# Kernel optimization log

Measured on AMD Instinct MI355X. Metric: run time of the kernel, lower is better.

Reference implementation:

```python
import jax, jax.numpy as jnp
import numpy as np

B, NODES, IN_DIM, OUT_DIM, CAPS, K, NUM_ROUTE = 32, 512, 256, 128, 16, 5, 3

def squash(s):
    # s: [..., out]; scale = |s|^2/(1+|s|^2), direction s/(|s|+eps)
    sn = jnp.sum(s * s, axis=-1, keepdims=True)
    return (sn / (1.0 + sn)) * s / (jnp.sqrt(sn) + 1e-8)

def setup_inputs() -> dict:
    key = jax.random.key(0)
    k1, k2, k3, k4 = jax.random.split(key, 4)
    return {
        "x": jax.random.normal(k1, (B, NODES, IN_DIM), jnp.float32),
        "contribution": jax.random.normal(k2, (B, NODES), jnp.float32),
        "W": jax.random.normal(k3, (K, IN_DIM, OUT_DIM), jnp.float32),
        "alpha": jax.random.normal(k4, (NODES, CAPS, K), jnp.float32),
    }

def reference(x, contribution, W, alpha):
    # per-node, per-capsule transform: sum_k alpha[n,c,k] * W[k,i,o] -> [nodes, caps, in, out]
    Wn = jnp.einsum('nck,kio->ncio', alpha, W)
    # prediction vectors u_hat: [B, caps, nodes, out]
    u_hat = jnp.einsum('bni,ncio->bcno', x, Wn)
    u_det = jax.lax.stop_gradient(u_hat)
    # routing logits b init from (detached) contribution: [B, caps, nodes, 1]
    b = jnp.broadcast_to(
        jax.lax.stop_gradient(contribution)[:, None, :, None],
        (x.shape[0], CAPS, x.shape[1], 1))
    for _ in range(NUM_ROUTE):
        c = jax.nn.softmax(b, axis=1)              # over capsule axis
        v = squash(jnp.sum(c * u_det, axis=2))     # [B, caps, out]
        b = b + jnp.einsum('bcno,bco->bcn', u_det, v)[..., None]
    c = jax.nn.softmax(b, axis=1)
    s = jnp.sum(c * u_hat, axis=2)                 # [B, caps, out] (non-detached)
    return squash(s)
```

## Files before the change

### kernel.cpp

```cpp
#include <hip/hip_runtime.h>
#include <math.h>

#define B_ 32
#define NODES_ 512
#define IN_ 256
#define OUT_ 128
#define CAPS_ 16
#define KW_ 5
#define M_ (B_*NODES_)
#define N_ (KW_*OUT_)
#define NCH 32

typedef __attribute__((ext_vector_type(8))) short short8;
typedef __attribute__((ext_vector_type(4))) float f32x4;

#define Y_BOFF   0
#define L_BOFF   41943040
#define V_BOFF   42991616
#define SP_BOFF  43253760
#define BT_SZ    (N_*IN_*2)

__device__ __forceinline__ float b2f(unsigned short u) {
  union { unsigned int i; float f; } c; c.i = ((unsigned int)u) << 16; return c.f;
}
__device__ __forceinline__ unsigned short f2b(float f) {
  union { float f; unsigned int i; } c; c.f = f;
  unsigned int u = c.i;
  u += 0x7fffu + ((u >> 16) & 1u);
  return (unsigned short)(u >> 16);
}
__device__ __forceinline__ void async_load16(const void* g, void* l) {
  __builtin_amdgcn_global_load_lds(
      (const __attribute__((address_space(1))) unsigned int*)g,
      (__attribute__((address_space(3))) unsigned int*)l, 16, 0, 0);
}

__global__ __launch_bounds__(256) void conv_w(const float* __restrict__ W,
                                              unsigned short* __restrict__ bThi,
                                              unsigned short* __restrict__ bTlo) {
  int n = blockIdx.x;
  int i = threadIdx.x;
  int k = n >> 7, o = n & 127;
  float v = W[((size_t)k*IN_ + i)*OUT_ + o];
  unsigned short h = f2b(v);
  size_t dst = ((size_t)(i >> 3)*N_ + n)*8 + (i & 7);
  bThi[dst] = h;
  bTlo[dst] = f2b(v - b2f(h));
}

__global__ __launch_bounds__(512) void gemm_fn(const float* __restrict__ x,
                                               const unsigned short* __restrict__ bThi,
                                               const unsigned short* __restrict__ bTlo,
                                               float* __restrict__ y) {
  __shared__ float A_lds[8*64*4];
  __shared__ short Bh_lds[4*640*8];
  __shared__ short Bl_lds[4*640*8];
  const int t    = threadIdx.x;
  const int w    = t >> 6;
  const int lane = t & 63;
  const int lrow = lane & 15;
  const int lk   = lane >> 4;
  const int m0   = blockIdx.x * 64;
  const int wn0  = w * 80;

  f32x4 acc[4][5];
  #pragma unroll
  for (int i=0;i<4;++i)
    #pragma unroll
    for (int j=0;j<5;++j) acc[i][j] = (f32x4){0.f,0.f,0.f,0.f};

  for (int kbi = 0; kbi < 8; ++kbi) {
    const int kb = kbi*32;
    async_load16(x + (size_t)(m0 + lane)*IN_ + kb + w*4, &A_lds[(w*64)*4]);
    const unsigned short* bh_src = bThi + (size_t)kbi*4*N_*8;
    const unsigned short* bl_src = bTlo + (size_t)kbi*4*N_*8;
    #pragma unroll
    for (int q=0; q<5; ++q) {
      int db = q*512 + w*64;
      async_load16(bh_src + (size_t)(db + lane)*8, &Bh_lds[db*8]);
      async_load16(bl_src + (size_t)(db + lane)*8, &Bl_lds[db*8]);
    }
    __syncthreads();

    short8 ah[4], al[4];
    #pragma unroll
    for (int mi=0; mi<4; ++mi) {
      int row = mi*16 + lrow;
      f32x4 a0 = *(const f32x4*)&A_lds[((2*lk  )*64 + row)*4];
      f32x4 a1 = *(const f32x4*)&A_lds[((2*lk+1)*64 + row)*4];
      #pragma unroll
      for (int j=0; j<8; ++j) {
        float f = (j < 4) ? a0[j] : a1[j-4];
        unsigned short h = f2b(f);
        ah[mi][j] = (short)h;
        al[mi][j] = (short)f2b(f - b2f(h));
      }
    }
    #pragma unroll
    for (int ni=0; ni<5; ++ni) {
      int nb = wn0 + ni*16 + lrow;
      short8 bh = *(const short8*)&Bh_lds[(lk*N_ + nb)*8];
      short8 bl = *(const short8*)&Bl_lds[(lk*N_ + nb)*8];
      #pragma unroll
      for (int mi=0; mi<4; ++mi) {
        acc[mi][ni] = __builtin_amdgcn_mfma_f32_16x16x32_bf16(bh, ah[mi], acc[mi][ni], 0, 0, 0);
        acc[mi][ni] = __builtin_amdgcn_mfma_f32_16x16x32_bf16(bh, al[mi], acc[mi][ni], 0, 0, 0);
        acc[mi][ni] = __builtin_amdgcn_mfma_f32_16x16x32_bf16(bl, ah[mi], acc[mi][ni], 0, 0, 0);
      }
    }
    __syncthreads();
  }

  #pragma unroll
  for (int mi=0; mi<4; ++mi) {
    int m = m0 + mi*16 + lrow;
    #pragma unroll
    for (int ni=0; ni<5; ++ni) {
      int nb = wn0 + ni*16 + lk*4;
      float4 o = {acc[mi][ni][0], acc[mi][ni][1], acc[mi][ni][2], acc[mi][ni][3]};
      *(float4*)(y + (size_t)m*N_ + nb) = o;
    }
  }
}

__global__ __launch_bounds__(256) void route_step(const float* __restrict__ y,
                                                  const float* __restrict__ alpha,
                                                  const float* __restrict__ contrib,
                                                  float* __restrict__ logits,
                                                  const float* __restrict__ vin,
                                                  float* __restrict__ s_part,
                                                  int mode) {
  __shared__ __align__(16) float sh_y[16*640];
  __shared__ __align__(16) float sh_v[16*132];
  __shared__ __align__(16) float sh_alpha[16*16*5];
  __shared__ float sh_logit[16][16];
  __shared__ float sh_cw[16][16];

  const int t  = threadIdx.x;
  const int ch = blockIdx.x;
  const int b  = blockIdx.y;
  const int n0 = ch*16;

  const float* ybase = y + ((size_t)(b*NODES_ + n0))*KW_*OUT_;
  #pragma unroll
  for (int q=0; q<10; ++q) {
    int d0 = q*256 + (t & ~63);
    async_load16(ybase + (size_t)(d0 + (t & 63))*4, &sh_y[d0*4]);
  }
  const float* abase = alpha + (size_t)n0*CAPS_*KW_;
  for (int i = t; i < 320; i += 256) {
    float4 av = *(const float4*)(abase + i*4);
    *(float4*)&sh_alpha[i*4] = av;
  }
  if (mode >= 1) {
    const float* vbase = vin + (size_t)b*CAPS_*OUT_;
    #pragma unroll
    for (int q=0; q<2; ++q) {
      int flat = (t + q*256)*4;
      int c = flat >> 7, o = flat & 127;
      float4 vv = *(const float4*)(vbase + flat);
      *(float4*)&sh_v[c*132 + o] = vv;
    }
    int node = t & 15, cap = t >> 4;
    sh_logit[node][cap] = logits[((size_t)b*CAPS_ + cap)*NODES_ + n0 + node];
  } else {
    int node = t & 15, cap = t >> 4;
    float cv = contrib[(size_t)b*NODES_ + n0 + node];
    sh_logit[node][cap] = cv;
    logits[((size_t)b*CAPS_ + cap)*NODES_ + n0 + node] = cv;
  }
  __syncthreads();

  if (mode >= 1) {
    int node = t >> 4, cap = t & 15;
    const float* al = &sh_alpha[(node*16+cap)*5];
    float a0=al[0],a1=al[1],a2=al[2],a3=al[3],a4=al[4];
    const float* yb = &sh_y[node*640];
    const float* vb = &sh_v[cap*132];
    float accd = 0.f;
    #pragma unroll 4
    for (int o=0; o<128; o+=4) {
      float4 y0 = *(const float4*)(yb + 0*128 + o);
      float4 y1 = *(const float4*)(yb + 1*128 + o);
      float4 y2 = *(const float4*)(yb + 2*128 + o);
      float4 y3 = *(const float4*)(yb + 3*128 + o);
      float4 y4 = *(const float4*)(yb + 4*128 + o);
      float4 vv = *(const float4*)(vb + o);
      float ux = a0*y0.x + a1*y1.x + a2*y2.x + a3*y3.x + a4*y4.x;
      float uy = a0*y0.y + a1*y1.y + a2*y2.y + a3*y3.y + a4*y4.y;
      float uz = a0*y0.z + a1*y1.z + a2*y2.z + a3*y3.z + a4*y4.z;
      float uw = a0*y0.w + a1*y1.w + a2*y2.w + a3*y3.w + a4*y4.w;
      accd += ux*vv.x + uy*vv.y + uz*vv.z + uw*vv.w;
    }
    float newl = sh_logit[node][cap] + accd;
    sh_logit[node][cap] = newl;
    logits[((size_t)b*CAPS_ + cap)*NODES_ + n0 + node] = newl;
    __syncthreads();
    if (t < 16) {
      int nd = t;
      float m = -1e30f;
      #pragma unroll
      for (int c=0;c<16;++c) m = fmaxf(m, sh_logit[nd][c]);
      float s = 0.f;
      float e[16];
      #pragma unroll
      for (int c=0;c<16;++c) { e[c] = __expf(sh_logit[nd][c]-m); s += e[c]; }
      float inv = 1.f/s;
      #pragma unroll
      for (int c=0;c<16;++c) sh_cw[nd][c] = e[c]*inv;
    }
  } else {
    int node = t >> 4, cap = t & 15;
    sh_cw[node][cap] = 1.f/16.f;
  }
  __syncthreads();

  float* spb = s_part + ((size_t)(b*NCH + ch))*CAPS_*OUT_;
  #pragma unroll
  for (int sl=0; sl<2; ++sl) {
    int slot = t + sl*256;
    int c  = slot & 15;
    int o  = (slot >> 4) * 4;
    float4 acc = {0.f,0.f,0.f,0.f};
    #pragma unroll 4
    for (int nd=0; nd<16; ++nd) {
      const float* al = &sh_alpha[(nd*16+c)*5];
      float a0=al[0],a1=al[1],a2=al[2],a3=al[3],a4=al[4];
      const float* yb = &sh_y[nd*640 + o];
      float4 y0 = *(const float4*)(yb);
      float4 y1 = *(const float4*)(yb + 128);
      float4 y2 = *(const float4*)(yb + 256);
      float4 y3 = *(const float4*)(yb + 384);
      float4 y4 = *(const float4*)(yb + 512);
      float cw = sh_cw[nd][c];
      acc.x += cw*(a0*y0.x + a1*y1.x + a2*y2.x + a3*y3.x + a4*y4.x);
      acc.y += cw*(a0*y0.y + a1*y1.y + a2*y2.y + a3*y3.y + a4*y4.y);
      acc.z += cw*(a0*y0.z + a1*y1.z + a2*y2.z + a3*y3.z + a4*y4.z);
      acc.w += cw*(a0*y0.w + a1*y1.w + a2*y2.w + a3*y3.w + a4*y4.w);
    }
    *(float4*)(spb + c*OUT_ + o) = acc;
  }
}

__global__ __launch_bounds__(128) void squash_k(const float* __restrict__ s_part,
                                                float* __restrict__ out) {
  const int bc = blockIdx.x;
  const int o  = threadIdx.x;
  const int b = bc >> 4, c = bc & 15;
  const float* sp = s_part + ((size_t)(b*NCH)*CAPS_ + c)*OUT_ + o;
  float s = 0.f;
  #pragma unroll
  for (int ch=0; ch<NCH; ++ch) s += sp[(size_t)ch*CAPS_*OUT_];
  float ss = s*s;
  #pragma unroll
  for (int off=32; off>0; off>>=1) ss += __shfl_down(ss, off, 64);
  __shared__ float red[2];
  if ((o & 63) == 0) red[o>>6] = ss;
  __syncthreads();
  float sn = red[0] + red[1];
  float scale = (sn/(1.f+sn)) / (sqrtf(sn)+1e-8f);
  out[(size_t)bc*OUT_ + o] = scale*s;
}

extern "C" void kernel_launch(void* const* d_in, const int* in_sizes, int n_in,
                              void* d_out, int out_size, void* d_ws, size_t ws_size,
                              hipStream_t stream) {
  const float* x       = (const float*)d_in[0];
  const float* contrib = (const float*)d_in[1];
  const float* W       = (const float*)d_in[2];
  const float* alpha   = (const float*)d_in[3];
  float* out = (float*)d_out;
  char*  wsb = (char*)d_ws;

  float* y             = (float*)(wsb + Y_BOFF);
  float* logits        = (float*)(wsb + L_BOFF);
  float* v             = (float*)(wsb + V_BOFF);
  float* s_part        = (float*)(wsb + SP_BOFF);
  unsigned short* bThi = (unsigned short*)(wsb + SP_BOFF);
  unsigned short* bTlo = (unsigned short*)(wsb + SP_BOFF + BT_SZ);

  conv_w<<<N_, 256, 0, stream>>>(W, bThi, bTlo);
  gemm_fn<<<M_/64, 512, 0, stream>>>(x, bThi, bTlo, y);

  route_step<<<dim3(NCH, B_), 256, 0, stream>>>(y, alpha, contrib, logits, v, s_part, 0);
  squash_k<<<B_*CAPS_, 128, 0, stream>>>(s_part, v);

  for (int it=0; it<3; ++it) {
    route_step<<<dim3(NCH, B_), 256, 0, stream>>>(y, alpha, contrib, logits, v, s_part, 1);
    squash_k<<<B_*CAPS_, 128, 0, stream>>>(s_part, (it==2) ? out : v);
  }
}
```

Measured before the change: 150.4 us.

## Process four node chunks per routing block with register-prefetched next chunk

The routing kernel now uses 512-thread blocks that each walk four 16-node chunks, prefetching the next chunk's y, alpha and logits into registers while the current chunk is computed from LDS. The y tile row stride is padded to avoid bank conflicts, and the logit dot product is split across two lanes joined with a shuffle. The GEMM's A tile load switches from async LDS loads to a plain coalesced float4 load and store. This aims to hide global load latency and raise per-block parallelism, at the cost of fewer blocks (256 versus 1024), more barriers per block and higher register pressure.

After: 195.6 us. 1.3x slower.

```diff
diff --git a/kernel.cpp b/kernel.cpp
--- a/kernel.cpp
+++ b/kernel.cpp
@@ -62,6 +62,8 @@
   const int lk   = lane >> 4;
   const int m0   = blockIdx.x * 64;
   const int wn0  = w * 80;
+  const int arow = t >> 3;
+  const int ac4  = t & 7;
 
   f32x4 acc[4][5];
   #pragma unroll
@@ -71,7 +73,6 @@
 
   for (int kbi = 0; kbi < 8; ++kbi) {
     const int kb = kbi*32;
-    async_load16(x + (size_t)(m0 + lane)*IN_ + kb + w*4, &A_lds[(w*64)*4]);
     const unsigned short* bh_src = bThi + (size_t)kbi*4*N_*8;
     const unsigned short* bl_src = bTlo + (size_t)kbi*4*N_*8;
     #pragma unroll
@@ -79,6 +80,10 @@
       int db = q*512 + w*64;
       async_load16(bh_src + (size_t)(db + lane)*8, &Bh_lds[db*8]);
       async_load16(bl_src + (size_t)(db + lane)*8, &Bl_lds[db*8]);
+    }
+    {
+      float4 av = *(const float4*)(x + (size_t)(m0 + arow)*IN_ + kb + ac4*4);
+      *(float4*)&A_lds[((ac4*64) + arow)*4] = av;
     }
     __syncthreads();
 
@@ -123,122 +128,145 @@
   }
 }
 
-__global__ __launch_bounds__(256) void route_step(const float* __restrict__ y,
-                                                  const float* __restrict__ alpha,
-                                                  const float* __restrict__ contrib,
-                                                  float* __restrict__ logits,
-                                                  const float* __restrict__ vin,
-                                                  float* __restrict__ s_part,
-                                                  int mode) {
-  __shared__ __align__(16) float sh_y[16*640];
+__global__ __launch_bounds__(512) void route4(const float* __restrict__ y,
+                                              const float* __restrict__ alpha,
+                                              const float* __restrict__ contrib,
+                                              float* __restrict__ logits,
+                                              const float* __restrict__ vin,
+                                              float* __restrict__ s_part,
+                                              int mode) {
+  __shared__ __align__(16) float sh_y[16*644];
   __shared__ __align__(16) float sh_v[16*132];
   __shared__ __align__(16) float sh_alpha[16*16*5];
   __shared__ float sh_logit[16][16];
   __shared__ float sh_cw[16][16];
 
-  const int t  = threadIdx.x;
-  const int ch = blockIdx.x;
-  const int b  = blockIdx.y;
-  const int n0 = ch*16;
-
-  const float* ybase = y + ((size_t)(b*NODES_ + n0))*KW_*OUT_;
-  #pragma unroll
-  for (int q=0; q<10; ++q) {
-    int d0 = q*256 + (t & ~63);
-    async_load16(ybase + (size_t)(d0 + (t & 63))*4, &sh_y[d0*4]);
-  }
-  const float* abase = alpha + (size_t)n0*CAPS_*KW_;
-  for (int i = t; i < 320; i += 256) {
-    float4 av = *(const float4*)(abase + i*4);
-    *(float4*)&sh_alpha[i*4] = av;
-  }
+  const int t = threadIdx.x;
+  const int g = blockIdx.x;
+  const int b = blockIdx.y;
+
   if (mode >= 1) {
-    const float* vbase = vin + (size_t)b*CAPS_*OUT_;
-    #pragma unroll
-    for (int q=0; q<2; ++q) {
-      int flat = (t + q*256)*4;
-      int c = flat >> 7, o = flat & 127;
-      float4 vv = *(const float4*)(vbase + flat);
-      *(float4*)&sh_v[c*132 + o] = vv;
-    }
-    int node = t & 15, cap = t >> 4;
-    sh_logit[node][cap] = logits[((size_t)b*CAPS_ + cap)*NODES_ + n0 + node];
-  } else {
-    int node = t & 15, cap = t >> 4;
-    float cv = contrib[(size_t)b*NODES_ + n0 + node];
-    sh_logit[node][cap] = cv;
-    logits[((size_t)b*CAPS_ + cap)*NODES_ + n0 + node] = cv;
-  }
-  __syncthreads();
-
-  if (mode >= 1) {
-    int node = t >> 4, cap = t & 15;
-    const float* al = &sh_alpha[(node*16+cap)*5];
-    float a0=al[0],a1=al[1],a2=al[2],a3=al[3],a4=al[4];
-    const float* yb = &sh_y[node*640];
-    const float* vb = &sh_v[cap*132];
-    float accd = 0.f;
-    #pragma unroll 4
-    for (int o=0; o<128; o+=4) {
-      float4 y0 = *(const float4*)(yb + 0*128 + o);
-      float4 y1 = *(const float4*)(yb + 1*128 + o);
-      float4 y2 = *(const float4*)(yb + 2*128 + o);
-      float4 y3 = *(const float4*)(yb + 3*128 + o);
-      float4 y4 = *(const float4*)(yb + 4*128 + o);
-      float4 vv = *(const float4*)(vb + o);
-      float ux = a0*y0.x + a1*y1.x + a2*y2.x + a3*y3.x + a4*y4.x;
-      float uy = a0*y0.y + a1*y1.y + a2*y2.y + a3*y3.y + a4*y4.y;
-      float uz = a0*y0.z + a1*y1.z + a2*y2.z + a3*y3.z + a4*y4.z;
-      float uw = a0*y0.w + a1*y1.w + a2*y2.w + a3*y3.w + a4*y4.w;
-      accd += ux*vv.x + uy*vv.y + uz*vv.z + uw*vv.w;
-    }
-    float newl = sh_logit[node][cap] + accd;
-    sh_logit[node][cap] = newl;
-    logits[((size_t)b*CAPS_ + cap)*NODES_ + n0 + node] = newl;
-    __syncthreads();
-    if (t < 16) {
-      int nd = t;
-      float m = -1e30f;
+    int flat = t*4;
+    float4 vv = *(const float4*)(vin + (size_t)b*CAPS_*OUT_ + flat);
+    *(float4*)&sh_v[(flat >> 7)*132 + (flat & 127)] = vv;
+  }
+
+  float4 yreg[5]; float4 areg = {0,0,0,0}; float lreg = 0.f;
+  {
+    int ch0 = g*4;
+    const float* yb0 = y + (size_t)(b*NODES_ + ch0*16)*N_;
+    #pragma unroll
+    for (int q=0;q<5;++q) yreg[q] = *(const float4*)(yb0 + (size_t)(t + q*512)*4);
+    if (t < 320) areg = *(const float4*)(alpha + (size_t)ch0*16*CAPS_*KW_ + (size_t)t*4);
+    if (t < 256) {
+      int node = t & 15, cap = t >> 4;
+      lreg = (mode >= 1) ? logits[((size_t)b*CAPS_ + cap)*NODES_ + ch0*16 + node]
+                         : contrib[(size_t)b*NODES_ + ch0*16 + node];
+    }
+  }
+
+  #pragma unroll
+  for (int i = 0; i < 4; ++i) {
+    const int ch = g*4 + i;
+    const int n0 = ch*16;
+
+    #pragma unroll
+    for (int q=0;q<5;++q) {
+      int flat = (t + q*512)*4;
+      int node = flat / 640;
+      int rem  = flat - node*640;
+      *(float4*)&sh_y[node*644 + rem] = yreg[q];
+    }
+    if (t < 320) *(float4*)&sh_alpha[t*4] = areg;
+    if (t < 256) {
+      int node = t & 15, cap = t >> 4;
+      sh_logit[node][cap] = lreg;
+      if (mode == 0) logits[((size_t)b*CAPS_ + cap)*NODES_ + n0 + node] = lreg;
+    }
+    __syncthreads();
+
+    if (i < 3) {
+      int ch2 = ch + 1;
+      const float* ybn = y + (size_t)(b*NODES_ + ch2*16)*N_;
       #pragma unroll
-      for (int c=0;c<16;++c) m = fmaxf(m, sh_logit[nd][c]);
-      float s = 0.f;
-      float e[16];
-      #pragma unroll
-      for (int c=0;c<16;++c) { e[c] = __expf(sh_logit[nd][c]-m); s += e[c]; }
-      float inv = 1.f/s;
-      #pragma unroll
-      for (int c=0;c<16;++c) sh_cw[nd][c] = e[c]*inv;
-    }
-  } else {
-    int node = t >> 4, cap = t & 15;
-    sh_cw[node][cap] = 1.f/16.f;
-  }
-  __syncthreads();
-
-  float* spb = s_part + ((size_t)(b*NCH + ch))*CAPS_*OUT_;
-  #pragma unroll
-  for (int sl=0; sl<2; ++sl) {
-    int slot = t + sl*256;
-    int c  = slot & 15;
-    int o  = (slot >> 4) * 4;
-    float4 acc = {0.f,0.f,0.f,0.f};
-    #pragma unroll 4
-    for (int nd=0; nd<16; ++nd) {
-      const float* al = &sh_alpha[(nd*16+c)*5];
+      for (int q=0;q<5;++q) yreg[q] = *(const float4*)(ybn + (size_t)(t + q*512)*4);
+      if (t < 320) areg = *(const float4*)(alpha + (size_t)ch2*16*CAPS_*KW_ + (size_t)t*4);
+      if (t < 256) {
+        int node = t & 15, cap = t >> 4;
+        lreg = (mode >= 1) ? logits[((size_t)b*CAPS_ + cap)*NODES_ + ch2*16 + node]
+                           : contrib[(size_t)b*NODES_ + ch2*16 + node];
+      }
+    }
+
+    if (mode >= 1) {
+      int nd = t >> 5, cap = (t >> 1) & 15, half = t & 1;
+      const float* al = &sh_alpha[(nd*16+cap)*5];
       float a0=al[0],a1=al[1],a2=al[2],a3=al[3],a4=al[4];
-      const float* yb = &sh_y[nd*640 + o];
-      float4 y0 = *(const float4*)(yb);
-      float4 y1 = *(const float4*)(yb + 128);
-      float4 y2 = *(const float4*)(yb + 256);
-      float4 y3 = *(const float4*)(yb + 384);
-      float4 y4 = *(const float4*)(yb + 512);
-      float cw = sh_cw[nd][c];
-      acc.x += cw*(a0*y0.x + a1*y1.x + a2*y2.x + a3*y3.x + a4*y4.x);
-      acc.y += cw*(a0*y0.y + a1*y1.y + a2*y2.y + a3*y3.y + a4*y4.y);
-      acc.z += cw*(a0*y0.z + a1*y1.z + a2*y2.z + a3*y3.z + a4*y4.z);
-      acc.w += cw*(a0*y0.w + a1*y1.w + a2*y2.w + a3*y3.w + a4*y4.w);
-    }
-    *(float4*)(spb + c*OUT_ + o) = acc;
+      const float* yb = &sh_y[nd*644] + half*64;
+      const float* vb = &sh_v[cap*132] + half*64;
+      float accd = 0.f;
+      #pragma unroll 4
+      for (int o=0; o<64; o+=4) {
+        float4 y0 = *(const float4*)(yb + 0*128 + o);
+        float4 y1 = *(const float4*)(yb + 1*128 + o);
+        float4 y2 = *(const float4*)(yb + 2*128 + o);
+        float4 y3 = *(const float4*)(yb + 3*128 + o);
+        float4 y4 = *(const float4*)(yb + 4*128 + o);
+        float4 vv = *(const float4*)(vb + o);
+        float ux = a0*y0.x + a1*y1.x + a2*y2.x + a3*y3.x + a4*y4.x;
+        float uy = a0*y0.y + a1*y1.y + a2*y2.y + a3*y3.y + a4*y4.y;
+        float uz = a0*y0.z + a1*y1.z + a2*y2.z + a3*y3.z + a4*y4.z;
+        float uw = a0*y0.w + a1*y1.w + a2*y2.w + a3*y3.w + a4*y4.w;
+        accd += ux*vv.x + uy*vv.y + uz*vv.z + uw*vv.w;
+      }
+      float tot = accd + __shfl_xor(accd, 1, 64);
+      if (half == 0) {
+        float newl = sh_logit[nd][cap] + tot;
+        sh_logit[nd][cap] = newl;
+        logits[((size_t)b*CAPS_ + cap)*NODES_ + n0 + nd] = newl;
+      }
+      __syncthreads();
+      if (t < 16) {
+        int nd2 = t;
+        float m = -1e30f;
+        #pragma unroll
+        for (int c=0;c<16;++c) m = fmaxf(m, sh_logit[nd2][c]);
+        float s = 0.f;
+        float e[16];
+        #pragma unroll
+        for (int c=0;c<16;++c) { e[c] = __expf(sh_logit[nd2][c]-m); s += e[c]; }
+        float inv = 1.f/s;
+        #pragma unroll
+        for (int c=0;c<16;++c) sh_cw[nd2][c] = e[c]*inv;
+      }
+    } else {
+      if (t < 256) sh_cw[t & 15][t >> 4] = 1.f/16.f;
+    }
+    __syncthreads();
+
+    {
+      int c = t & 15;
+      int o = (t >> 4) * 4;
+      float4 acc = {0.f,0.f,0.f,0.f};
+      #pragma unroll 4
+      for (int nd=0; nd<16; ++nd) {
+        const float* al = &sh_alpha[(nd*16+c)*5];
+        float a0=al[0],a1=al[1],a2=al[2],a3=al[3],a4=al[4];
+        const float* yb = &sh_y[nd*644 + o];
+        float4 y0 = *(const float4*)(yb);
+        float4 y1 = *(const float4*)(yb + 128);
+        float4 y2 = *(const float4*)(yb + 256);
+        float4 y3 = *(const float4*)(yb + 384);
+        float4 y4 = *(const float4*)(yb + 512);
+        float cw = sh_cw[nd][c];
+        acc.x += cw*(a0*y0.x + a1*y1.x + a2*y2.x + a3*y3.x + a4*y4.x);
+        acc.y += cw*(a0*y0.y + a1*y1.y + a2*y2.y + a3*y3.y + a4*y4.y);
+        acc.z += cw*(a0*y0.z + a1*y1.z + a2*y2.z + a3*y3.z + a4*y4.z);
+        acc.w += cw*(a0*y0.w + a1*y1.w + a2*y2.w + a3*y3.w + a4*y4.w);
+      }
+      *(float4*)(s_part + ((size_t)(b*NCH + ch)*CAPS_ + c)*OUT_ + o) = acc;
+    }
+    __syncthreads();
   }
 }
 
@@ -282,11 +310,11 @@
   conv_w<<<N_, 256, 0, stream>>>(W, bThi, bTlo);
   gemm_fn<<<M_/64, 512, 0, stream>>>(x, bThi, bTlo, y);
 
-  route_step<<<dim3(NCH, B_), 256, 0, stream>>>(y, alpha, contrib, logits, v, s_part, 0);
+  route4<<<dim3(8, B_), 512, 0, stream>>>(y, alpha, contrib, logits, v, s_part, 0);
   squash_k<<<B_*CAPS_, 128, 0, stream>>>(s_part, v);
 
   for (int it=0; it<3; ++it) {
-    route_step<<<dim3(NCH, B_), 256, 0, stream>>>(y, alpha, contrib, logits, v, s_part, 1);
+    route4<<<dim3(8, B_), 512, 0, stream>>>(y, alpha, contrib, logits, v, s_part, 1);
     squash_k<<<B_*CAPS_, 128, 0, stream>>>(s_part, (it==2) ? out : v);
   }
 }
```

## Pad routing LDS layouts, restructure logit dot per node, and use plain A loads

Applied to the files above, without the earlier changes.

The GEMM now loads the x tile with ordinary vector global loads and LDS stores instead of async global-to-LDS loads. The routing kernel pads the y and alpha tiles in LDS to cut bank conflicts and stages y through registers. It also rewrites the logit-update dot product so each node's 16 threads split the output dimension, compute all 16 capsules, and combine partial sums with wave shuffles. This removes the strided per-capsule LDS access at the cost of more registers and shuffle traffic, and the softmax weights reuse the logit buffer.

After: 151.4 us. About the same (+0.7%).

```diff
diff --git a/kernel.cpp b/kernel.cpp
--- a/kernel.cpp
+++ b/kernel.cpp
@@ -19,6 +19,9 @@
 #define V_BOFF   42991616
 #define SP_BOFF  43253760
 #define BT_SZ    (N_*IN_*2)
+
+#define YPAD 648
+#define APAD 84
 
 __device__ __forceinline__ float b2f(unsigned short u) {
   union { unsigned int i; float f; } c; c.i = ((unsigned int)u) << 16; return c.f;
@@ -62,6 +65,8 @@
   const int lk   = lane >> 4;
   const int m0   = blockIdx.x * 64;
   const int wn0  = w * 80;
+  const int arow = t >> 3;
+  const int ac4  = t & 7;
 
   f32x4 acc[4][5];
   #pragma unroll
@@ -71,7 +76,6 @@
 
   for (int kbi = 0; kbi < 8; ++kbi) {
     const int kb = kbi*32;
-    async_load16(x + (size_t)(m0 + lane)*IN_ + kb + w*4, &A_lds[(w*64)*4]);
     const unsigned short* bh_src = bThi + (size_t)kbi*4*N_*8;
     const unsigned short* bl_src = bTlo + (size_t)kbi*4*N_*8;
     #pragma unroll
@@ -79,6 +83,10 @@
       int db = q*512 + w*64;
       async_load16(bh_src + (size_t)(db + lane)*8, &Bh_lds[db*8]);
       async_load16(bl_src + (size_t)(db + lane)*8, &Bl_lds[db*8]);
+    }
+    {
+      float4 av = *(const float4*)(x + (size_t)(m0 + arow)*IN_ + kb + ac4*4);
+      *(float4*)&A_lds[((ac4*64) + arow)*4] = av;
     }
     __syncthreads();
 
@@ -130,27 +138,34 @@
                                                   const float* __restrict__ vin,
                                                   float* __restrict__ s_part,
                                                   int mode) {
-  __shared__ __align__(16) float sh_y[16*640];
+  __shared__ __align__(16) float sh_y[16*YPAD];
   __shared__ __align__(16) float sh_v[16*132];
-  __shared__ __align__(16) float sh_alpha[16*16*5];
+  __shared__ __align__(16) float sh_alpha[16*APAD];
   __shared__ float sh_logit[16][16];
-  __shared__ float sh_cw[16][16];
 
   const int t  = threadIdx.x;
   const int ch = blockIdx.x;
   const int b  = blockIdx.y;
   const int n0 = ch*16;
 
-  const float* ybase = y + ((size_t)(b*NODES_ + n0))*KW_*OUT_;
+  const float* ybase = y + ((size_t)(b*NODES_ + n0))*N_;
+  float4 yst[10];
+  #pragma unroll
+  for (int q=0; q<10; ++q) yst[q] = *(const float4*)(ybase + (size_t)(t + q*256)*4);
   #pragma unroll
   for (int q=0; q<10; ++q) {
-    int d0 = q*256 + (t & ~63);
-    async_load16(ybase + (size_t)(d0 + (t & 63))*4, &sh_y[d0*4]);
+    int flat = (t + q*256)*4;
+    int nd   = flat / 640;
+    int rem  = flat - nd*640;
+    *(float4*)&sh_y[nd*YPAD + rem] = yst[q];
   }
   const float* abase = alpha + (size_t)n0*CAPS_*KW_;
   for (int i = t; i < 320; i += 256) {
     float4 av = *(const float4*)(abase + i*4);
-    *(float4*)&sh_alpha[i*4] = av;
+    int flat = i*4;
+    int nd   = flat / 80;
+    int rem  = flat - nd*80;
+    *(float4*)&sh_alpha[nd*APAD + rem] = av;
   }
   if (mode >= 1) {
     const float* vbase = vin + (size_t)b*CAPS_*OUT_;
@@ -161,57 +176,65 @@
       float4 vv = *(const float4*)(vbase + flat);
       *(float4*)&sh_v[c*132 + o] = vv;
     }
-    int node = t & 15, cap = t >> 4;
-    sh_logit[node][cap] = logits[((size_t)b*CAPS_ + cap)*NODES_ + n0 + node];
+    int nd = t & 15, cap = t >> 4;
+    sh_logit[nd][cap] = logits[((size_t)b*CAPS_ + cap)*NODES_ + n0 + nd];
   } else {
-    int node = t & 15, cap = t >> 4;
-    float cv = contrib[(size_t)b*NODES_ + n0 + node];
-    sh_logit[node][cap] = cv;
-    logits[((size_t)b*CAPS_ + cap)*NODES_ + n0 + node] = cv;
+    int nd = t >> 4, cap = t & 15;
+    logits[((size_t)b*CAPS_ + cap)*NODES_ + n0 + nd] = contrib[(size_t)b*NODES_ + n0 + nd];
   }
   __syncthreads();
 
   if (mode >= 1) {
-    int node = t >> 4, cap = t & 15;
-    const float* al = &sh_alpha[(node*16+cap)*5];
-    float a0=al[0],a1=al[1],a2=al[2],a3=al[3],a4=al[4];
-    const float* yb = &sh_y[node*640];
-    const float* vb = &sh_v[cap*132];
-    float accd = 0.f;
-    #pragma unroll 4
-    for (int o=0; o<128; o+=4) {
-      float4 y0 = *(const float4*)(yb + 0*128 + o);
-      float4 y1 = *(const float4*)(yb + 1*128 + o);
-      float4 y2 = *(const float4*)(yb + 2*128 + o);
-      float4 y3 = *(const float4*)(yb + 3*128 + o);
-      float4 y4 = *(const float4*)(yb + 4*128 + o);
-      float4 vv = *(const float4*)(vb + o);
-      float ux = a0*y0.x + a1*y1.x + a2*y2.x + a3*y3.x + a4*y4.x;
-      float uy = a0*y0.y + a1*y1.y + a2*y2.y + a3*y3.y + a4*y4.y;
-      float uz = a0*y0.z + a1*y1.z + a2*y2.z + a3*y3.z + a4*y4.z;
-      float uw = a0*y0.w + a1*y1.w + a2*y2.w + a3*y3.w + a4*y4.w;
-      accd += ux*vv.x + uy*vv.y + uz*vv.z + uw*vv.w;
-    }
-    float newl = sh_logit[node][cap] + accd;
-    sh_logit[node][cap] = newl;
-    logits[((size_t)b*CAPS_ + cap)*NODES_ + n0 + node] = newl;
+    const int node = t >> 4, s = t & 15;
+    float ar[16][5];
+    #pragma unroll
+    for (int c=0;c<16;++c)
+      #pragma unroll
+      for (int k=0;k<5;++k) ar[c][k] = sh_alpha[node*APAD + c*5 + k];
+    float acc16[16];
+    #pragma unroll
+    for (int c=0;c<16;++c) acc16[c] = 0.f;
+    const float* yb = &sh_y[node*YPAD];
+    #pragma unroll
+    for (int j=0;j<8;++j) {
+      int o = s + 16*j;
+      float y0=yb[o], y1=yb[128+o], y2=yb[256+o], y3=yb[384+o], y4=yb[512+o];
+      #pragma unroll
+      for (int c=0;c<16;++c) {
+        float u = ar[c][0]*y0 + ar[c][1]*y1 + ar[c][2]*y2 + ar[c][3]*y3 + ar[c][4]*y4;
+        acc16[c] += u * sh_v[c*132 + o];
+      }
+    }
+    #pragma unroll
+    for (int c=0;c<16;++c) {
+      acc16[c] += __shfl_xor(acc16[c], 1, 64);
+      acc16[c] += __shfl_xor(acc16[c], 2, 64);
+      acc16[c] += __shfl_xor(acc16[c], 4, 64);
+      acc16[c] += __shfl_xor(acc16[c], 8, 64);
+    }
+    float mine = 0.f;
+    #pragma unroll
+    for (int c=0;c<16;++c) mine = (s == c) ? acc16[c] : mine;
+    float newl = sh_logit[node][s] + mine;
+    sh_logit[node][s] = newl;
+    logits[((size_t)b*CAPS_ + s)*NODES_ + n0 + node] = newl;
     __syncthreads();
     if (t < 16) {
       int nd = t;
       float m = -1e30f;
       #pragma unroll
       for (int c=0;c<16;++c) m = fmaxf(m, sh_logit[nd][c]);
-      float s = 0.f;
+      float ssum = 0.f;
       float e[16];
       #pragma unroll
-      for (int c=0;c<16;++c) { e[c] = __expf(sh_logit[nd][c]-m); s += e[c]; }
-      float inv = 1.f/s;
-      #pragma unroll
-      for (int c=0;c<16;++c) sh_cw[nd][c] = e[c]*inv;
+      for (int c=0;c<16;++c) { e[c] = __expf(sh_logit[nd][c]-m); ssum += e[c]; }
+      float inv = 1.f/ssum;
+      #pragma unroll
+      for (int c=0;c<16;++c) sh_logit[nd][c] = e[c]*inv;
     }
   } else {
-    int node = t >> 4, cap = t & 15;
-    sh_cw[node][cap] = 1.f/16.f;
+    int nd = t >> 4, cap = t & 15;
+    sh_logit[nd][cap] = 1.f/16.f;
   }
   __syncthreads();
 
@@ -224,15 +247,15 @@
     float4 acc = {0.f,0.f,0.f,0.f};
     #pragma unroll 4
     for (int nd=0; nd<16; ++nd) {
-      const float* al = &sh_alpha[(nd*16+c)*5];
+      const float* al = &sh_alpha[nd*APAD + c*5];
       float a0=al[0],a1=al[1],a2=al[2],a3=al[3],a4=al[4];
-      const float* yb = &sh_y[nd*640 + o];
+      const float* yb = &sh_y[nd*YPAD + o];
       float4 y0 = *(const float4*)(yb);
       float4 y1 = *(const float4*)(yb + 128);
       float4 y2 = *(const float4*)(yb + 256);
       float4 y3 = *(const float4*)(yb + 384);
       float4 y4 = *(const float4*)(yb + 512);
-      float cw = sh_cw[nd][c];
+      float cw = sh_logit[nd][c];
       acc.x += cw*(a0*y0.x + a1*y1.x + a2*y2.x + a3*y3.x + a4*y4.x);
       acc.y += cw*(a0*y0.y + a1*y1.y + a2*y2.y + a3*y3.y + a4*y4.y);
       acc.z += cw*(a0*y0.z + a1*y1.z + a2*y2.z + a3*y3.z + a4*y4.z);
```

## Read y directly from global in routing, drop LDS staging, pad alpha

Applied to the files above, without the earlier changes.

The routing kernel stops staging the 40KB per-block y tile in LDS and reads y straight from global memory (through cache) in both the logit-update and the weighted-sum phases. This frees LDS to allow more resident blocks. The alpha LDS layout gets padding, and the softmax weights reuse the logit array. The GEMM also replaces the async global-to-LDS load of the A tile with a plain vectorised load and store using a transposed thread mapping. The cost is repeated global or L2 traffic for y, and possibly uncoalesced reads in the dot-product phase.

New measurement: 198.8 us. 1.32x slower.

```diff
diff --git a/kernel.cpp b/kernel.cpp
--- a/kernel.cpp
+++ b/kernel.cpp
@@ -19,6 +19,8 @@
 #define V_BOFF   42991616
 #define SP_BOFF  43253760
 #define BT_SZ    (N_*IN_*2)
+
+#define APAD 84
 
 __device__ __forceinline__ float b2f(unsigned short u) {
   union { unsigned int i; float f; } c; c.i = ((unsigned int)u) << 16; return c.f;
@@ -62,6 +64,8 @@
   const int lk   = lane >> 4;
   const int m0   = blockIdx.x * 64;
   const int wn0  = w * 80;
+  const int arow = t >> 3;
+  const int ac4  = t & 7;
 
   f32x4 acc[4][5];
   #pragma unroll
@@ -71,7 +75,6 @@
 
   for (int kbi = 0; kbi < 8; ++kbi) {
     const int kb = kbi*32;
-    async_load16(x + (size_t)(m0 + lane)*IN_ + kb + w*4, &A_lds[(w*64)*4]);
     const unsigned short* bh_src = bThi + (size_t)kbi*4*N_*8;
     const unsigned short* bl_src = bTlo + (size_t)kbi*4*N_*8;
     #pragma unroll
@@ -79,6 +82,10 @@
       int db = q*512 + w*64;
       async_load16(bh_src + (size_t)(db + lane)*8, &Bh_lds[db*8]);
       async_load16(bl_src + (size_t)(db + lane)*8, &Bl_lds[db*8]);
+    }
+    {
+      float4 av = *(const float4*)(x + (size_t)(m0 + arow)*IN_ + kb + ac4*4);
+      *(float4*)&A_lds[((ac4*64) + arow)*4] = av;
     }
     __syncthreads();
 
@@ -130,27 +137,22 @@
                                                   const float* __restrict__ vin,
                                                   float* __restrict__ s_part,
                                                   int mode) {
-  __shared__ __align__(16) float sh_y[16*640];
   __shared__ __align__(16) float sh_v[16*132];
-  __shared__ __align__(16) float sh_alpha[16*16*5];
+  __shared__ __align__(16) float sh_alpha[16*APAD];
   __shared__ float sh_logit[16][16];
-  __shared__ float sh_cw[16][16];
 
   const int t  = threadIdx.x;
   const int ch = blockIdx.x;
   const int b  = blockIdx.y;
   const int n0 = ch*16;
 
-  const float* ybase = y + ((size_t)(b*NODES_ + n0))*KW_*OUT_;
-  #pragma unroll
-  for (int q=0; q<10; ++q) {
-    int d0 = q*256 + (t & ~63);
-    async_load16(ybase + (size_t)(d0 + (t & 63))*4, &sh_y[d0*4]);
-  }
   const float* abase = alpha + (size_t)n0*CAPS_*KW_;
   for (int i = t; i < 320; i += 256) {
     float4 av = *(const float4*)(abase + i*4);
-    *(float4*)&sh_alpha[i*4] = av;
+    int flat = i*4;
+    int nd   = flat / 80;
+    int rem  = flat - nd*80;
+    *(float4*)&sh_alpha[nd*APAD + rem] = av;
   }
   if (mode >= 1) {
     const float* vbase = vin + (size_t)b*CAPS_*OUT_;
@@ -161,21 +163,19 @@
       float4 vv = *(const float4*)(vbase + flat);
       *(float4*)&sh_v[c*132 + o] = vv;
     }
-    int node = t & 15, cap = t >> 4;
-    sh_logit[node][cap] = logits[((size_t)b*CAPS_ + cap)*NODES_ + n0 + node];
+    int nd = t & 15, cap = t >> 4;
+    sh_logit[nd][cap] = logits[((size_t)b*CAPS_ + cap)*NODES_ + n0 + nd];
   } else {
-    int node = t & 15, cap = t >> 4;
-    float cv = contrib[(size_t)b*NODES_ + n0 + node];
-    sh_logit[node][cap] = cv;
-    logits[((size_t)b*CAPS_ + cap)*NODES_ + n0 + node] = cv;
+    int nd = t >> 4, cap = t & 15;
+    logits[((size_t)b*CAPS_ + cap)*NODES_ + n0 + nd] = contrib[(size_t)b*NODES_ + n0 + nd];
   }
   __syncthreads();
 
   if (mode >= 1) {
     int node = t >> 4, cap = t & 15;
-    const float* al = &sh_alpha[(node*16+cap)*5];
+    const float* al = &sh_alpha[node*APAD + cap*5];
     float a0=al[0],a1=al[1],a2=al[2],a3=al[3],a4=al[4];
-    const float* yb = &sh_y[node*640];
+    const float* yb = y + (size_t)(b*NODES_ + n0 + node)*N_;
     const float* vb = &sh_v[cap*132];
     float accd = 0.f;
     #pragma unroll 4
@@ -201,21 +201,22 @@
       float m = -1e30f;
       #pragma unroll
       for (int c=0;c<16;++c) m = fmaxf(m, sh_logit[nd][c]);
-      float s = 0.f;
+      float ssum = 0.f;
       float e[16];
       #pragma unroll
-      for (int c=0;c<16;++c) { e[c] = __expf(sh_logit[nd][c]-m); s += e[c]; }
-      float inv = 1.f/s;
-      #pragma unroll
-      for (int c=0;c<16;++c) sh_cw[nd][c] = e[c]*inv;
+      for (int c=0;c<16;++c) { e[c] = __expf(sh_logit[nd][c]-m); ssum += e[c]; }
+      float inv = 1.f/ssum;
+      #pragma unroll
+      for (int c=0;c<16;++c) sh_logit[nd][c] = e[c]*inv;
     }
   } else {
-    int node = t >> 4, cap = t & 15;
-    sh_cw[node][cap] = 1.f/16.f;
+    int nd = t >> 4, cap = t & 15;
+    sh_logit[nd][cap] = 1.f/16.f;
   }
   __syncthreads();
 
   float* spb = s_part + ((size_t)(b*NCH + ch))*CAPS_*OUT_;
+  const float* ychunk = y + (size_t)(b*NODES_ + n0)*N_;
   #pragma unroll
   for (int sl=0; sl<2; ++sl) {
     int slot = t + sl*256;
@@ -224,15 +225,15 @@
     float4 acc = {0.f,0.f,0.f,0.f};
     #pragma unroll 4
     for (int nd=0; nd<16; ++nd) {
-      const float* al = &sh_alpha[(nd*16+c)*5];
+      const float* al = &sh_alpha[nd*APAD + c*5];
       float a0=al[0],a1=al[1],a2=al[2],a3=al[3],a4=al[4];
-      const float* yb = &sh_y[nd*640 + o];
+      const float* yb = ychunk + (size_t)nd*N_ + o;
       float4 y0 = *(const float4*)(yb);
       float4 y1 = *(const float4*)(yb + 128);
       float4 y2 = *(const float4*)(yb + 256);
       float4 y3 = *(const float4*)(yb + 384);
       float4 y4 = *(const float4*)(yb + 512);
-      float cw = sh_cw[nd][c];
+      float cw = sh_logit[nd][c];
       acc.x += cw*(a0*y0.x + a1*y1.x + a2*y2.x + a3*y3.x + a4*y4.x);
       acc.y += cw*(a0*y0.y + a1*y1.y + a2*y2.y + a3*y3.y + a4*y4.y);
       acc.z += cw*(a0*y0.z + a1*y1.z + a2*y2.z + a3*y3.z + a4*y4.z);
```
